# Kernel optimization log

Measured on AMD Instinct MI355X. Metric: run time of the kernel, lower is better.

The kernel has to match this reference:

```python
import jax, jax.numpy as jnp
import numpy as np
import math

B, T, C, H, D = 2, 2048, 768, 12, 64


def _rms_norm(x):
    # torch F.rms_norm with eps=None -> finfo(dtype).eps, no learned weight
    eps = jnp.finfo(x.dtype).eps
    return x * jax.lax.rsqrt(jnp.mean(x * x, axis=-1, keepdims=True) + eps)


def _apply_rotary(x, cos, sin):
    # nanochat rotary: split head_dim into halves
    d = x.shape[-1] // 2
    x1, x2 = x[..., :d], x[..., d:]
    return jnp.concatenate([x1 * cos + x2 * sin, -x1 * sin + x2 * cos], axis=-1)


def setup_inputs() -> dict:
    key = jax.random.key(0)
    ks = jax.random.split(key, 8)
    s = 0.02
    x = jax.random.normal(ks[0], (B, T, C), jnp.float32)
    cos = jax.random.normal(ks[1], (1, T, 1, D // 2), jnp.float32)
    sin = jax.random.normal(ks[2], (1, T, 1, D // 2), jnp.float32)
    Wq = jax.random.normal(ks[3], (C, C), jnp.float32) * s
    Wk = jax.random.normal(ks[4], (C, C), jnp.float32) * s
    Wv = jax.random.normal(ks[5], (C, C), jnp.float32) * s
    Wo = jax.random.normal(ks[6], (C, C), jnp.float32) * s
    beta = jnp.ones((H,), jnp.float32) * 0.5
    return {"x": x, "cos": cos, "sin": sin, "Wq": Wq, "Wk": Wk, "Wv": Wv, "Wo": Wo, "beta": beta}


def reference(x, cos, sin, Wq, Wk, Wv, Wo, beta):
    b, t, c = x.shape
    h = beta.shape[0]
    d = c // h
    q = (x @ Wq.T).reshape(b, t, h, d)
    k = (x @ Wk.T).reshape(b, t, h, d)
    v = (x @ Wv.T).reshape(b, t, h, d)
    q = _rms_norm(_apply_rotary(q, cos, sin)).transpose(0, 2, 1, 3)  # (B,H,T,D)
    k = _rms_norm(_apply_rotary(k, cos, sin)).transpose(0, 2, 1, 3)
    v = v.transpose(0, 2, 1, 3)
    # phase coherence: mean over RoPE frequencies of cos(position_diff * theta)
    pos = jnp.arange(t, dtype=jnp.float32)
    theta = 10000.0 ** (-jnp.arange(0, d, 2, dtype=jnp.float32) / d)  # (D/2,)
    pdiff = pos[None, :] - pos[:, None]  # (T,T); cos is even so orientation is irrelevant
    coh_base = jnp.mean(jnp.cos(pdiff[:, :, None] * theta), axis=-1)  # (T,T)
    coherence = 1.0 + beta[None, :, None, None] * coh_base[None, None, :, :]  # (1,H,T,T)
    scores = jnp.einsum('bhqd,bhkd->bhqk', q, k) / math.sqrt(d)
    scores = scores * coherence
    w = jax.nn.softmax(scores, axis=-1)
    causal = jnp.tril(jnp.ones((t, t), dtype=bool))
    w = w * causal[None, None, :, :]
    w = w / (jnp.sum(w, axis=-1, keepdims=True) + 1e-8)
    y = jnp.einsum('bhqk,bhkd->bhqd', w, v)
    y = y.transpose(0, 2, 1, 3).reshape(b, t, c)
    return y @ Wo.T
```

## Files before the change

kernel.cpp:

```cpp
#include <hip/hip_runtime.h>
#include <hip/hip_bf16.h>
#include <math.h>

#define B_ 2
#define T_ 2048
#define C_ 768
#define H_ 12
#define D_ 64

typedef __attribute__((ext_vector_type(8))) short short8;
typedef __attribute__((ext_vector_type(4))) float f32x4;
typedef __attribute__((ext_vector_type(16))) float f32x16;

template <bool V> struct BoolC { static constexpr bool value = V; };

#define SBAR() do { asm volatile("" ::: "memory"); __builtin_amdgcn_s_barrier(); asm volatile("" ::: "memory"); } while (0)
#define WAITVM(N) asm volatile("s_waitcnt vmcnt(" #N ")" ::: "memory")

__device__ inline unsigned short f2bf(float f) {
    unsigned int x = __float_as_uint(f);
    unsigned int r = x + 0x7FFFu + ((x >> 16) & 1u);
    return (unsigned short)(r >> 16);
}

__device__ __forceinline__ unsigned cvtpk(float lo, float hi) {
    unsigned r;
    asm("v_cvt_pk_bf16_f32 %0, %1, %2" : "=v"(r) : "v"(lo), "v"(hi));
    return r;
}

__device__ __forceinline__ void plswap(unsigned& a, unsigned& b) {
    asm volatile("v_permlane32_swap_b32 %0, %1" : "+v"(a), "+v"(b));
}

__device__ __forceinline__ void gll16(const void* g, void* l) {
    __builtin_amdgcn_global_load_lds(
        (const __attribute__((address_space(1))) unsigned int*)g,
        (__attribute__((address_space(3))) unsigned int*)l, 16, 0, 0);
}

__global__ __launch_bounds__(256) void convert_all_kernel(const float* __restrict__ x,
                                                          const float* __restrict__ Wq,
                                                          const float* __restrict__ Wk,
                                                          const float* __restrict__ Wv,
                                                          const float* __restrict__ Wo,
                                                          unsigned short* __restrict__ xb,
                                                          unsigned short* __restrict__ wqkv,
                                                          unsigned short* __restrict__ wob,
                                                          float* __restrict__ coh) {
    if (blockIdx.x >= 5376) {
        int dd = (blockIdx.x - 5376) * 256 + threadIdx.x;
        if (dd < T_) {
            float s = 0.f;
            for (int m = 0; m < 32; ++m) {
                float theta = powf(10000.f, -(float)m / 32.f);
                s += cosf((float)dd * theta);
            }
            coh[dd] = s * (1.f / 32.f);
        }
        return;
    }
    int i = blockIdx.x * 256 + threadIdx.x;
    float4 v;
    ushort4* d;
    if (i < 786432) {
        v = ((const float4*)x)[i];
        d = (ushort4*)xb + i;
    } else {
        int wI = i - 786432;
        int widx = wI / 147456;
        int off = wI - widx * 147456;
        const float* W = widx == 0 ? Wq : widx == 1 ? Wk : widx == 2 ? Wv : Wo;
        v = ((const float4*)W)[off];
        unsigned short* base = (widx == 3) ? wob : (wqkv + widx * 589824);
        d = (ushort4*)base + off;
    }
    ushort4 o;
    o.x = f2bf(v.x); o.y = f2bf(v.y); o.z = f2bf(v.z); o.w = f2bf(v.w);
    *d = o;
}

union QkvSmem {
    struct { unsigned short A[2][128][32]; unsigned short Bm[2][128][32]; } g;
    unsigned short tr[4][64][72];
};

__global__ __launch_bounds__(256) void gemm_qkv_kernel(const unsigned short* __restrict__ xb,
                                                       const unsigned short* __restrict__ wqkv,
                                                       const float* __restrict__ cosb,
                                                       const float* __restrict__ sinb,
                                                       unsigned short* __restrict__ qbf,
                                                       unsigned short* __restrict__ kbf,
                                                       unsigned short* __restrict__ vt) {
    __shared__ QkvSmem sm;

    int bm = blockIdx.x, tn = blockIdx.y;
    int tid = threadIdx.x;
    int w = tid >> 6, lane = tid & 63;
    int rc = lane & 15, kg = lane >> 4;
    int wr = w >> 1, wc = w & 1;

    const unsigned short* ga = xb + (size_t)(bm * 128 + w * 32 + (lane >> 2)) * 768 + (lane & 3) * 8;
    const unsigned short* gb = wqkv + (size_t)(tn * 128 + w * 32 + (lane >> 2)) * 768 + (lane & 3) * 8;

    f32x4 acc[4][4];
    #pragma unroll
    for (int i = 0; i < 4; ++i)
        #pragma unroll
        for (int j = 0; j < 4; ++j) acc[i][j] = (f32x4){0.f, 0.f, 0.f, 0.f};

    auto stageg = [&](int buf, int k0) {
        gll16(ga + k0, &sm.g.A[buf][w * 32][0]);
        gll16(ga + k0 + 16 * 768, &sm.g.A[buf][w * 32 + 16][0]);
        gll16(gb + k0, &sm.g.Bm[buf][w * 32][0]);
        gll16(gb + k0 + 16 * 768, &sm.g.Bm[buf][w * 32 + 16][0]);
    };
    auto comp = [&](int buf) {
        short8 aF[4], bF[4];
        #pragma unroll
        for (int ai = 0; ai < 4; ++ai) aF[ai] = *(const short8*)&sm.g.A[buf][wr * 64 + ai * 16 + rc][kg * 8];
        #pragma unroll
        for (int bj = 0; bj < 4; ++bj) bF[bj] = *(const short8*)&sm.g.Bm[buf][wc * 64 + bj * 16 + rc][kg * 8];
        __builtin_amdgcn_s_setprio(1);
        #pragma unroll
        for (int ai = 0; ai < 4; ++ai)
            #pragma unroll
            for (int bj = 0; bj < 4; ++bj)
                acc[ai][bj] = __builtin_amdgcn_mfma_f32_16x16x32_bf16(aF[ai], bF[bj], acc[ai][bj], 0, 0, 0);
        __builtin_amdgcn_s_setprio(0);
    };

    stageg(0, 0);
    __syncthreads();
    for (int kk = 0; kk < 23; ++kk) {
        stageg((kk + 1) & 1, (kk + 1) * 32);
        WAITVM(4);
        SBAR();
        comp(kk & 1);
        SBAR();
    }
    WAITVM(0);
    SBAR();
    comp(1);
    __syncthreads();

    int hg = tn * 2 + wc;
    int tensor = hg / 12;
    int h = hg % 12;

    if (tensor < 2) {
        float scale = tensor == 0 ? 0.125f : 1.0f;
        unsigned short* dst = (tensor == 0 ? qbf : kbf);
        #pragma unroll
        for (int ai = 0; ai < 4; ++ai) {
            #pragma unroll
            for (int rr = 0; rr < 4; ++rr) {
                int m = bm * 128 + wr * 64 + ai * 16 + kg * 4 + rr;
                int b = m >> 11, t = m & 2047;
                float c0 = cosb[t * 32 + rc], c1 = cosb[t * 32 + 16 + rc];
                float s0 = sinb[t * 32 + rc], s1 = sinb[t * 32 + 16 + rc];
                float x0 = acc[ai][0][rr], x1 = acc[ai][1][rr];
                float x2 = acc[ai][2][rr], x3 = acc[ai][3][rr];
                float o0 = x0 * c0 + x2 * s0;
                float o1 = x1 * c1 + x3 * s1;
                float o2 = -x0 * s0 + x2 * c0;
                float o3 = -x1 * s1 + x3 * c1;
                float ss = o0 * o0 + o1 * o1 + o2 * o2 + o3 * o3;
                ss += __shfl_xor(ss, 1); ss += __shfl_xor(ss, 2);
                ss += __shfl_xor(ss, 4); ss += __shfl_xor(ss, 8);
                float rn = rsqrtf(ss * (1.f / 64.f) + 1.1920929e-07f) * scale;
                unsigned short* dp = dst + (((size_t)b * H_ + h) * T_ + t) * 64;
                dp[rc]      = f2bf(o0 * rn);
                dp[16 + rc] = f2bf(o1 * rn);
                dp[32 + rc] = f2bf(o2 * rn);
                dp[48 + rc] = f2bf(o3 * rn);
            }
        }
    } else {
        #pragma unroll
        for (int ai = 0; ai < 4; ++ai)
            #pragma unroll
            for (int bj = 0; bj < 4; ++bj)
                #pragma unroll
                for (int rr = 0; rr < 4; ++rr)
                    sm.tr[w][bj * 16 + rc][ai * 16 + kg * 4 + rr] = f2bf(acc[ai][bj][rr]);
    }
    __syncthreads();
    if (tensor == 2) {
        int m0 = bm * 128 + wr * 64;
        int b = m0 >> 11, t0 = m0 & 2047;
        int d = lane;
        unsigned short* gp = vt + (((size_t)b * H_ + h) * 64 + d) * T_ + t0;
        const uint4* src = (const uint4*)&sm.tr[w][d][0];
        #pragma unroll
        for (int i = 0; i < 8; ++i) ((uint4*)gp)[i] = src[i];
    }
}

__global__ __launch_bounds__(256) void gemm_out_kernel(const unsigned short* __restrict__ A,
                                                       const unsigned short* __restrict__ Bw,
                                                       float* __restrict__ C) {
    __shared__ unsigned short lA[2][128][32];
    __shared__ unsigned short lB[2][64][32];
    int bm = blockIdx.x, tn = blockIdx.y;
    int tid = threadIdx.x;
    int w = tid >> 6, lane = tid & 63;
    int rc = lane & 15, kg = lane >> 4;
    int wr = w >> 1, wc = w & 1;

    const unsigned short* ga = A + (size_t)(bm * 128 + w * 32 + (lane >> 2)) * 768 + (lane & 3) * 8;
    const unsigned short* gbB = Bw + (size_t)(tn * 64 + w * 16 + (lane >> 2)) * 768 + (lane & 3) * 8;

    f32x4 acc[4][2];
    #pragma unroll
    for (int i = 0; i < 4; ++i)
        #pragma unroll
        for (int j = 0; j < 2; ++j) acc[i][j] = (f32x4){0.f, 0.f, 0.f, 0.f};

    auto stageg = [&](int buf, int k0) {
        gll16(ga + k0, &lA[buf][w * 32][0]);
        gll16(ga + k0 + 16 * 768, &lA[buf][w * 32 + 16][0]);
        gll16(gbB + k0, &lB[buf][w * 16][0]);
    };
    auto comp = [&](int buf) {
        short8 aF[4], bF[2];
        #pragma unroll
        for (int ai = 0; ai < 4; ++ai) aF[ai] = *(const short8*)&lA[buf][wr * 64 + ai * 16 + rc][kg * 8];
        #pragma unroll
        for (int bj = 0; bj < 2; ++bj) bF[bj] = *(const short8*)&lB[buf][wc * 32 + bj * 16 + rc][kg * 8];
        __builtin_amdgcn_s_setprio(1);
        #pragma unroll
        for (int ai = 0; ai < 4; ++ai)
            #pragma unroll
            for (int bj = 0; bj < 2; ++bj)
                acc[ai][bj] = __builtin_amdgcn_mfma_f32_16x16x32_bf16(aF[ai], bF[bj], acc[ai][bj], 0, 0, 0);
        __builtin_amdgcn_s_setprio(0);
    };

    stageg(0, 0);
    __syncthreads();
    for (int kk = 0; kk < 23; ++kk) {
        stageg((kk + 1) & 1, (kk + 1) * 32);
        WAITVM(3);
        SBAR();
        comp(kk & 1);
        SBAR();
    }
    WAITVM(0);
    SBAR();
    comp(1);

    #pragma unroll
    for (int ai = 0; ai < 4; ++ai)
        #pragma unroll
        for (int rr = 0; rr < 4; ++rr) {
            int m = bm * 128 + wr * 64 + ai * 16 + kg * 4 + rr;
            #pragma unroll
            for (int bj = 0; bj < 2; ++bj)
                C[(size_t)m * 768 + tn * 64 + wc * 32 + bj * 16 + rc] = acc[ai][bj][rr];
        }
}

__global__ __launch_bounds__(256) void attn_flash_kernel(const unsigned short* __restrict__ qbf,
                                                         const unsigned short* __restrict__ kbf,
                                                         const unsigned short* __restrict__ vt,
                                                         const float* __restrict__ coh,
                                                         const float* __restrict__ beta,
                                                         unsigned short* __restrict__ yb) {
    __shared__ unsigned short kT[2][64][64];
    __shared__ unsigned short vT[2][64][64];
    __shared__ float cfl[T_];

    int p = blockIdx.x;
    int xcd = p & 7, kk = p >> 3;
    int bl = kk >> 5, jsl = kk & 31;
    int bh = xcd * 3 + bl;
    int jj = (bl == 0) ? jsl : (bl == 1 ? (31 - jsl) : ((jsl * 5 + 3) & 31));
    int tq = 31 - jj;
    int b = bh / H_, h = bh % H_;

    int tid = threadIdx.x;
    int w = tid >> 6, lane = tid & 63;
    int qs = w >> 1, js = w & 1;
    int ql = lane & 31, hl = lane >> 5;

    float bv = beta[h];
    for (int i = tid; i < T_; i += 256)
        cfl[i] = (1.f + bv * coh[i]) * 1.4426950408889634f;

    int qb = tq * 64;
    const unsigned short* kb = kbf + (size_t)bh * T_ * 64;
    const unsigned short* vb = vt + (size_t)bh * 64 * T_;

    const unsigned short* qrow = qbf + ((size_t)bh * T_ + qb + qs * 32 + ql) * 64 + hl * 8;
    short8 qf[4];
    #pragma unroll
    for (int d = 0; d < 4; ++d) qf[d] = *(const short8*)(qrow + d * 16);

    f32x16 acc0, acc1;
    #pragma unroll
    for (int i = 0; i < 16; ++i) { acc0[i] = 0.f; acc1[i] = 0.f; }
    float z = 0.f;

    int Rk = js * 32 + ql;
    int kby[4];
    #pragma unroll
    for (int d = 0; d < 4; ++d) kby[d] = Rk * 128 + (((d * 2 + hl) ^ (Rk & 7)) << 4);
    int vby0[2], vby1[2];
    #pragma unroll
    for (int ks = 0; ks < 2; ++ks) {
        int Rv0 = ql, Rv1 = 32 + ql;
        vby0[ks] = Rv0 * 128 + (((js * 4 + ks * 2 + hl) ^ (Rv0 & 7)) << 4);
        vby1[ks] = Rv1 * 128 + (((js * 4 + ks * 2 + hl) ^ (Rv1 & 7)) << 4);
    }
    const char* kbase = (const char*)&kT[0][0][0];
    const char* vbase = (const char*)&vT[0][0][0];

    int rloc = lane >> 3;
    int gsw = ((lane & 7) ^ rloc) * 8;
    int r0 = w * 16;

    auto stage = [&](int buf, int tj) {
        gll16(kb + (size_t)(tj + r0 + rloc) * 64 + gsw,      &kT[buf][r0][0]);
        gll16(kb + (size_t)(tj + r0 + 8 + rloc) * 64 + gsw,  &kT[buf][r0 + 8][0]);
        gll16(vb + (size_t)(r0 + rloc) * T_ + tj + gsw,      &vT[buf][r0][0]);
        gll16(vb + (size_t)(r0 + 8 + rloc) * T_ + tj + gsw,  &vT[buf][r0 + 8][0]);
    };

    int qpos = qb + qs * 32 + ql;

    auto body = [&](int buf, int tj, auto maskc) {
        constexpr bool M = decltype(maskc)::value;
        f32x16 s;
        #pragma unroll
        for (int i = 0; i < 16; ++i) s[i] = 0.f;
        const char* kp = kbase + buf * 8192;
        __builtin_amdgcn_s_setprio(1);
        #pragma unroll
        for (int d = 0; d < 4; ++d) {
            short8 kf = *(const short8*)(kp + kby[d]);
            s = __builtin_amdgcn_mfma_f32_32x32x16_bf16(kf, qf[d], s, 0, 0, 0);
        }
        __builtin_amdgcn_s_setprio(0);
        int base = qpos - tj - js * 32 - 4 * hl;
        float e[16];
        #pragma unroll
        for (int r = 0; r < 16; ++r) {
            int dd = base - ((r & 3) + 8 * (r >> 2));
            if constexpr (M) {
                float ex = __builtin_amdgcn_exp2f(s[r] * cfl[dd < 0 ? 0 : dd]);
                e[r] = dd >= 0 ? ex : 0.f;
            } else {
                e[r] = __builtin_amdgcn_exp2f(s[r] * cfl[dd]);
            }
            z += e[r];
        }
        unsigned A0 = cvtpk(e[0], e[1]),  B0 = cvtpk(e[2], e[3]);
        unsigned C0 = cvtpk(e[4], e[5]),  D0 = cvtpk(e[6], e[7]);
        unsigned E0 = cvtpk(e[8], e[9]),  F0 = cvtpk(e[10], e[11]);
        unsigned G0 = cvtpk(e[12], e[13]), H0 = cvtpk(e[14], e[15]);
        plswap(A0, C0); plswap(B0, D0); plswap(E0, G0); plswap(F0, H0);
        union U { unsigned u[4]; short8 s8; };
        U p0, p1;
        p0.u[0] = A0; p0.u[1] = B0; p0.u[2] = C0; p0.u[3] = D0;
        p1.u[0] = E0; p1.u[1] = F0; p1.u[2] = G0; p1.u[3] = H0;
        const char* vp = vbase + buf * 8192;
        short8 v00 = *(const short8*)(vp + vby0[0]);
        short8 v01 = *(const short8*)(vp + vby0[1]);
        short8 v10 = *(const short8*)(vp + vby1[0]);
        short8 v11 = *(const short8*)(vp + vby1[1]);
        __builtin_amdgcn_s_setprio(1);
        acc0 = __builtin_amdgcn_mfma_f32_32x32x16_bf16(v00, p0.s8, acc0, 0, 0, 0);
        acc0 = __builtin_amdgcn_mfma_f32_32x32x16_bf16(v01, p1.s8, acc0, 0, 0, 0);
        acc1 = __builtin_amdgcn_mfma_f32_32x32x16_bf16(v10, p0.s8, acc1, 0, 0, 0);
        acc1 = __builtin_amdgcn_mfma_f32_32x32x16_bf16(v11, p1.s8, acc1, 0, 0, 0);
        __builtin_amdgcn_s_setprio(0);
    };

    int nt = tq + 1;
    stage(0, 0);
    __syncthreads();
    int cur = 0;
    for (int it = 0; it < nt - 1; ++it) {
        stage(cur ^ 1, (it + 1) * 64);
        WAITVM(4);
        SBAR();
        body(cur, it * 64, BoolC<false>{});
        SBAR();
        cur ^= 1;
    }
    WAITVM(0);
    SBAR();
    if (qs > js)      body(cur, (nt - 1) * 64, BoolC<false>{});
    else if (qs == js) body(cur, (nt - 1) * 64, BoolC<true>{});
    __syncthreads();

    z += __shfl_xor(z, 32);
    float* osc = (float*)&kT[0][0][0];
    float* zbuf = (float*)&vT[0][0][0];
    if (js == 0) {
        float* o = osc + qs * 2048;
        #pragma unroll
        for (int r = 0; r < 16; ++r) {
            o[r * 64 + lane] = acc0[r];
            o[(16 + r) * 64 + lane] = acc1[r];
        }
        if (lane < 32) zbuf[qs * 32 + ql] = z;
    }
    __syncthreads();
    if (js == 1) {
        float zt = z + zbuf[qs * 32 + ql];
        float invz = 1.f / zt;
        const float* o = osc + qs * 2048;
        #pragma unroll
        for (int r = 0; r < 16; ++r) {
            acc0[r] = (acc0[r] + o[r * 64 + lane]) * invz;
            acc1[r] = (acc1[r] + o[(16 + r) * 64 + lane]) * invz;
        }
        int t = qb + qs * 32 + ql;
        unsigned short* yp = yb + (((size_t)b * T_ + t) * H_ + h) * 64;
        #pragma unroll
        for (int g = 0; g < 4; ++g) {
            uint2 st0, st1;
            st0.x = cvtpk(acc0[g * 4 + 0], acc0[g * 4 + 1]);
            st0.y = cvtpk(acc0[g * 4 + 2], acc0[g * 4 + 3]);
            *(uint2*)(yp + g * 8 + 4 * hl) = st0;
            st1.x = cvtpk(acc1[g * 4 + 0], acc1[g * 4 + 1]);
            st1.y = cvtpk(acc1[g * 4 + 2], acc1[g * 4 + 3]);
            *(uint2*)(yp + 32 + g * 8 + 4 * hl) = st1;
        }
    }
}

extern "C" void kernel_launch(void* const* d_in, const int* in_sizes, int n_in,
                              void* d_out, int out_size, void* d_ws, size_t ws_size,
                              hipStream_t stream) {
    const float* x    = (const float*)d_in[0];
    const float* cosb = (const float*)d_in[1];
    const float* sinb = (const float*)d_in[2];
    const float* Wq   = (const float*)d_in[3];
    const float* Wk   = (const float*)d_in[4];
    const float* Wv   = (const float*)d_in[5];
    const float* Wo   = (const float*)d_in[6];
    const float* beta = (const float*)d_in[7];
    float* out = (float*)d_out;

    char* ws = (char*)d_ws;
    unsigned short* xb   = (unsigned short*)(ws + 0);
    unsigned short* wqkv = (unsigned short*)(ws + 6291456);
    unsigned short* wob  = (unsigned short*)(ws + 9830400);
    unsigned short* qbf  = (unsigned short*)(ws + 11010048);
    unsigned short* kbf  = (unsigned short*)(ws + 17301504);
    unsigned short* vt   = (unsigned short*)(ws + 23592960);
    unsigned short* yb   = (unsigned short*)(ws + 29884416);
    float*          coh  = (float*)(ws + 36175872);

    convert_all_kernel<<<5384, 256, 0, stream>>>(x, Wq, Wk, Wv, Wo, xb, wqkv, wob, coh);

    dim3 gq(32, 18);
    gemm_qkv_kernel<<<gq, 256, 0, stream>>>(xb, wqkv, cosb, sinb, qbf, kbf, vt);

    attn_flash_kernel<<<B_ * H_ * (T_ / 64), 256, 0, stream>>>(qbf, kbf, vt, coh, beta, yb);

    dim3 go(32, 12);
    gemm_out_kernel<<<go, 256, 0, stream>>>(yb, wob, out);
}
```

Measured before the change: 106.4 us.

## Shrink GEMM tiles to raise block count and add occupancy launch bounds

The QKV projection GEMM moves from 128x128 tiles to 128x64 tiles, one head per block, with each wave owning 32 rows. The V transpose epilogue is rewritten as a single shared 64x136 tile with coalesced stores. The output GEMM drops from 128x64 to 64x64 tiles, and all three main kernels get launch_bounds(256,4). The aim is to double the grid size so more workgroups fill the 256 CUs, and to improve occupancy. The cost is less operand reuse per block and more global loads overall.

```diff
diff --git a/kernel.cpp b/kernel.cpp
--- a/kernel.cpp
+++ b/kernel.cpp
@@ -81,49 +81,47 @@
 }
 
 union QkvSmem {
-    struct { unsigned short A[2][128][32]; unsigned short Bm[2][128][32]; } g;
-    unsigned short tr[4][64][72];
+    struct { unsigned short A[2][128][32]; unsigned short Bm[2][64][32]; } g;
+    unsigned short tr[64][136];
 };
 
-__global__ __launch_bounds__(256) void gemm_qkv_kernel(const unsigned short* __restrict__ xb,
-                                                       const unsigned short* __restrict__ wqkv,
-                                                       const float* __restrict__ cosb,
-                                                       const float* __restrict__ sinb,
-                                                       unsigned short* __restrict__ qbf,
-                                                       unsigned short* __restrict__ kbf,
-                                                       unsigned short* __restrict__ vt) {
+__global__ __launch_bounds__(256, 4) void gemm_qkv_kernel(const unsigned short* __restrict__ xb,
+                                                          const unsigned short* __restrict__ wqkv,
+                                                          const float* __restrict__ cosb,
+                                                          const float* __restrict__ sinb,
+                                                          unsigned short* __restrict__ qbf,
+                                                          unsigned short* __restrict__ kbf,
+                                                          unsigned short* __restrict__ vt) {
     __shared__ QkvSmem sm;
 
     int bm = blockIdx.x, tn = blockIdx.y;
     int tid = threadIdx.x;
     int w = tid >> 6, lane = tid & 63;
     int rc = lane & 15, kg = lane >> 4;
-    int wr = w >> 1, wc = w & 1;
 
     const unsigned short* ga = xb + (size_t)(bm * 128 + w * 32 + (lane >> 2)) * 768 + (lane & 3) * 8;
-    const unsigned short* gb = wqkv + (size_t)(tn * 128 + w * 32 + (lane >> 2)) * 768 + (lane & 3) * 8;
-
-    f32x4 acc[4][4];
-    #pragma unroll
-    for (int i = 0; i < 4; ++i)
+    const unsigned short* gb = wqkv + (size_t)(tn * 64 + w * 16 + (lane >> 2)) * 768 + (lane & 3) * 8;
+
+    f32x4 acc[2][4];
+    #pragma unroll
+    for (int i = 0; i < 2; ++i)
         #pragma unroll
         for (int j = 0; j < 4; ++j) acc[i][j] = (f32x4){0.f, 0.f, 0.f, 0.f};
 
     auto stageg = [&](int buf, int k0) {
         gll16(ga + k0, &sm.g.A[buf][w * 32][0]);
         gll16(ga + k0 + 16 * 768, &sm.g.A[buf][w * 32 + 16][0]);
-        gll16(gb + k0, &sm.g.Bm[buf][w * 32][0]);
-        gll16(gb + k0 + 16 * 768, &sm.g.Bm[buf][w * 32 + 16][0]);
+        gll16(gb + k0, &sm.g.Bm[buf][w * 16][0]);
     };
     auto comp = [&](int buf) {
-        short8 aF[4], bF[4];
-        #pragma unroll
-        for (int ai = 0; ai < 4; ++ai) aF[ai] = *(const short8*)&sm.g.A[buf][wr * 64 + ai * 16 + rc][kg * 8];
-        #pragma unroll
-        for (int bj = 0; bj < 4; ++bj) bF[bj] = *(const short8*)&sm.g.Bm[buf][wc * 64 + bj * 16 + rc][kg * 8];
+        short8 aF[2], bF[4];
+        #pragma unroll
+        for (int ai = 0; ai < 2; ++ai) aF[ai] = *(const short8*)&sm.g.A[buf][w * 32 + ai * 16 + rc][kg * 8];
+        #pragma unroll
+        for (int bj = 0; bj < 4; ++bj) bF[bj] = *(const short8*)&sm.g.Bm[buf][bj * 16 + rc][kg * 8];
         __builtin_amdgcn_s_setprio(1);
         #pragma unroll
-        for (int ai = 0; ai < 4; ++ai)
+        for (int ai = 0; ai < 2; ++ai)
             #pragma unroll
             for (int bj = 0; bj < 4; ++bj)
                 acc[ai][bj] = __builtin_amdgcn_mfma_f32_16x16x32_bf16(aF[ai], bF[bj], acc[ai][bj], 0, 0, 0);
@@ -134,7 +132,7 @@
     __syncthreads();
     for (int kk = 0; kk < 23; ++kk) {
         stageg((kk + 1) & 1, (kk + 1) * 32);
-        WAITVM(4);
+        WAITVM(3);
         SBAR();
         comp(kk & 1);
         SBAR();
@@ -144,18 +142,17 @@
     comp(1);
     __syncthreads();
 
-    int hg = tn * 2 + wc;
-    int tensor = hg / 12;
-    int h = hg % 12;
+    int tensor = tn / 12;
+    int h = tn % 12;
 
     if (tensor < 2) {
         float scale = tensor == 0 ? 0.125f : 1.0f;
         unsigned short* dst = (tensor == 0 ? qbf : kbf);
         #pragma unroll
-        for (int ai = 0; ai < 4; ++ai) {
+        for (int ai = 0; ai < 2; ++ai) {
             #pragma unroll
             for (int rr = 0; rr < 4; ++rr) {
-                int m = bm * 128 + wr * 64 + ai * 16 + kg * 4 + rr;
+                int m = bm * 128 + w * 32 + ai * 16 + kg * 4 + rr;
                 int b = m >> 11, t = m & 2047;
                 float c0 = cosb[t * 32 + rc], c1 = cosb[t * 32 + 16 + rc];
                 float s0 = sinb[t * 32 + rc], s1 = sinb[t * 32 + 16 + rc];
@@ -178,29 +175,28 @@
         }
     } else {
         #pragma unroll
-        for (int ai = 0; ai < 4; ++ai)
+        for (int ai = 0; ai < 2; ++ai)
             #pragma unroll
             for (int bj = 0; bj < 4; ++bj)
                 #pragma unroll
                 for (int rr = 0; rr < 4; ++rr)
-                    sm.tr[w][bj * 16 + rc][ai * 16 + kg * 4 + rr] = f2bf(acc[ai][bj][rr]);
-    }
-    __syncthreads();
-    if (tensor == 2) {
-        int m0 = bm * 128 + wr * 64;
+                    sm.tr[bj * 16 + rc][w * 32 + ai * 16 + kg * 4 + rr] = f2bf(acc[ai][bj][rr]);
+        __syncthreads();
+        int m0 = bm * 128;
         int b = m0 >> 11, t0 = m0 & 2047;
-        int d = lane;
-        unsigned short* gp = vt + (((size_t)b * H_ + h) * 64 + d) * T_ + t0;
-        const uint4* src = (const uint4*)&sm.tr[w][d][0];
-        #pragma unroll
-        for (int i = 0; i < 8; ++i) ((uint4*)gp)[i] = src[i];
-    }
-}
-
-__global__ __launch_bounds__(256) void gemm_out_kernel(const unsigned short* __restrict__ A,
-                                                       const unsigned short* __restrict__ Bw,
-                                                       float* __restrict__ C) {
-    __shared__ unsigned short lA[2][128][32];
+        int d = w * 16 + (lane >> 2);
+        int tl = (lane & 3) * 32;
+        unsigned short* gp = vt + (((size_t)b * H_ + h) * 64 + d) * T_ + t0 + tl;
+        #pragma unroll
+        for (int i = 0; i < 4; ++i)
+            *(uint4*)(gp + i * 8) = *(const uint4*)&sm.tr[d][tl + i * 8];
+    }
+}
+
+__global__ __launch_bounds__(256, 4) void gemm_out_kernel(const unsigned short* __restrict__ A,
+                                                          const unsigned short* __restrict__ Bw,
+                                                          float* __restrict__ C) {
+    __shared__ unsigned short lA[2][64][32];
     __shared__ unsigned short lB[2][64][32];
     int bm = blockIdx.x, tn = blockIdx.y;
     int tid = threadIdx.x;
@@ -208,29 +204,28 @@
     int rc = lane & 15, kg = lane >> 4;
     int wr = w >> 1, wc = w & 1;
 
-    const unsigned short* ga = A + (size_t)(bm * 128 + w * 32 + (lane >> 2)) * 768 + (lane & 3) * 8;
+    const unsigned short* ga = A + (size_t)(bm * 64 + w * 16 + (lane >> 2)) * 768 + (lane & 3) * 8;
     const unsigned short* gbB = Bw + (size_t)(tn * 64 + w * 16 + (lane >> 2)) * 768 + (lane & 3) * 8;
 
-    f32x4 acc[4][2];
-    #pragma unroll
-    for (int i = 0; i < 4; ++i)
+    f32x4 acc[2][2];
+    #pragma unroll
+    for (int i = 0; i < 2; ++i)
         #pragma unroll
         for (int j = 0; j < 2; ++j) acc[i][j] = (f32x4){0.f, 0.f, 0.f, 0.f};
 
     auto stageg = [&](int buf, int k0) {
-        gll16(ga + k0, &lA[buf][w * 32][0]);
-        gll16(ga + k0 + 16 * 768, &lA[buf][w * 32 + 16][0]);
+        gll16(ga + k0, &lA[buf][w * 16][0]);
         gll16(gbB + k0, &lB[buf][w * 16][0]);
     };
     auto comp = [&](int buf) {
-        short8 aF[4], bF[2];
-        #pragma unroll
-        for (int ai = 0; ai < 4; ++ai) aF[ai] = *(const short8*)&lA[buf][wr * 64 + ai * 16 + rc][kg * 8];
+        short8 aF[2], bF[2];
+        #pragma unroll
+        for (int ai = 0; ai < 2; ++ai) aF[ai] = *(const short8*)&lA[buf][wr * 32 + ai * 16 + rc][kg * 8];
         #pragma unroll
         for (int bj = 0; bj < 2; ++bj) bF[bj] = *(const short8*)&lB[buf][wc * 32 + bj * 16 + rc][kg * 8];
         __builtin_amdgcn_s_setprio(1);
         #pragma unroll
-        for (int ai = 0; ai < 4; ++ai)
+        for (int ai = 0; ai < 2; ++ai)
             #pragma unroll
             for (int bj = 0; bj < 2; ++bj)
                 acc[ai][bj] = __builtin_amdgcn_mfma_f32_16x16x32_bf16(aF[ai], bF[bj], acc[ai][bj], 0, 0, 0);
@@ -241,7 +236,7 @@
     __syncthreads();
     for (int kk = 0; kk < 23; ++kk) {
         stageg((kk + 1) & 1, (kk + 1) * 32);
-        WAITVM(3);
+        WAITVM(2);
         SBAR();
         comp(kk & 1);
         SBAR();
@@ -251,22 +246,22 @@
     comp(1);
 
     #pragma unroll
-    for (int ai = 0; ai < 4; ++ai)
+    for (int ai = 0; ai < 2; ++ai)
         #pragma unroll
         for (int rr = 0; rr < 4; ++rr) {
-            int m = bm * 128 + wr * 64 + ai * 16 + kg * 4 + rr;
+            int m = bm * 64 + wr * 32 + ai * 16 + kg * 4 + rr;
             #pragma unroll
             for (int bj = 0; bj < 2; ++bj)
                 C[(size_t)m * 768 + tn * 64 + wc * 32 + bj * 16 + rc] = acc[ai][bj][rr];
         }
 }
 
-__global__ __launch_bounds__(256) void attn_flash_kernel(const unsigned short* __restrict__ qbf,
-                                                         const unsigned short* __restrict__ kbf,
-                                                         const unsigned short* __restrict__ vt,
-                                                         const float* __restrict__ coh,
-                                                         const float* __restrict__ beta,
-                                                         unsigned short* __restrict__ yb) {
+__global__ __launch_bounds__(256, 4) void attn_flash_kernel(const unsigned short* __restrict__ qbf,
+                                                            const unsigned short* __restrict__ kbf,
+                                                            const unsigned short* __restrict__ vt,
+                                                            const float* __restrict__ coh,
+                                                            const float* __restrict__ beta,
+                                                            unsigned short* __restrict__ yb) {
     __shared__ unsigned short kT[2][64][64];
     __shared__ unsigned short vT[2][64][64];
     __shared__ float cfl[T_];
@@ -457,11 +452,11 @@
 
     convert_all_kernel<<<5384, 256, 0, stream>>>(x, Wq, Wk, Wv, Wo, xb, wqkv, wob, coh);
 
-    dim3 gq(32, 18);
+    dim3 gq(32, 36);
     gemm_qkv_kernel<<<gq, 256, 0, stream>>>(xb, wqkv, cosb, sinb, qbf, kbf, vt);
 
     attn_flash_kernel<<<B_ * H_ * (T_ / 64), 256, 0, stream>>>(qbf, kbf, vt, coh, beta, yb);
 
-    dim3 go(32, 12);
+    dim3 go(64, 12);
     gemm_out_kernel<<<go, 256, 0, stream>>>(yb, wob, out);
 }
```

New measurement: 98.01 us. 1.09x faster.
